# Kernel optimization log

Measured on AMD Instinct MI355X. Metric: run time of the kernel, lower is better.

## Reference

```python
import jax, jax.numpy as jnp
import numpy as np


def setup_inputs() -> dict:
    key = jax.random.key(0)
    k1, k2, k3, k4 = jax.random.split(key, 4)
    B, H, W, C, NCLS = 128, 14, 14, 512, 200
    # post-ReLU-like non-negative feature map
    x = jax.random.uniform(k1, (B, H, W, C), dtype=jnp.float32)
    # one-hot-like logits for ground-truth labels (only argmax is used)
    gt = jax.random.normal(k2, (B, NCLS), dtype=jnp.float32)
    # positional template codebook; index [H, W] (== shape[0]-1) is the sentinel
    # 'negative' template used for all-zero channels
    t_p = jax.random.normal(k3, (H + 1, W + 1, H, W), dtype=jnp.float32)
    # per-class channel template, broadcast-multiplied with masked features
    class_templates = jax.random.uniform(k4, (NCLS, H, W, C), dtype=jnp.float32)
    return {"x": x, "gt": gt, "t_p": t_p, "class_templates": class_templates}


def reference(x, gt, t_p, class_templates):
    # x: [B, H, W, C] channels-last feature map
    B, H, W, C = x.shape
    flat = x.reshape(B, H * W, C)
    # global spatial argmax per (batch, channel) == max_pool_with_argmax over full extent
    idx = jnp.argmax(flat, axis=1)            # [B, C]
    h = idx // W                               # [B, C]
    w = idx % W                                # [B, C]
    # channels whose spatial max is exactly 0 get the sentinel template index
    empty = jnp.max(flat, axis=1) == 0.0       # [B, C]
    sentinel = t_p.shape[0] - 1
    h = jnp.where(empty, sentinel, h)
    w = jnp.where(empty, sentinel, w)
    # gather positional templates: [B, C, H, W] -> [B, H, W, C]
    templates = jnp.transpose(t_p[h, w], (0, 2, 3, 1))
    masked = jax.nn.relu(x * templates)
    # training branch with gt, reduce_loss=False: mask by the class template
    cls = jnp.argmax(gt, axis=1)               # [B]
    masked = masked * class_templates[cls]     # [B, H, W, C]
    return (masked, x, templates)
```

## Files before the change

kernel.cpp:

```cpp
#include <hip/hip_runtime.h>

#define B    128
#define H    14
#define W    14
#define C    512
#define NCLS 200
#define HW   (H * W)
#define TP_DIM 15
#define SENT_OFF ((14 * TP_DIM + 14) * HW)

typedef float  v4f __attribute__((ext_vector_type(4)));
typedef int    v4i __attribute__((ext_vector_type(4)));

__global__ __launch_bounds__(512) void fused_kernel(
        const float* __restrict__ x,
        const float* __restrict__ gt,
        const float* __restrict__ t_p,
        const float* __restrict__ ctpl,
        float*       __restrict__ out) {
    __shared__ int s_off[C];
    __shared__ int s_cls;

    const int tid  = threadIdx.x;
    const int b    = blockIdx.x >> 1;
    const int half = blockIdx.x & 1;

    {
        const float* xp = x + (size_t)b * HW * C + tid;
        float best = xp[0];
        int   bs   = 0;
#pragma unroll 13
        for (int s = 1; s < HW; ++s) {
            float v = xp[(size_t)s * C];
            if (v > best) { best = v; bs = s; }
        }
        int off;
        if (best == 0.0f) {
            off = SENT_OFF;
        } else {
            int h = bs / W;
            int w = bs - h * W;
            off = (h * TP_DIM + w) * HW;
        }
        s_off[tid] = off;
    }

    if (tid < 64) {
        const float* g = gt + (size_t)b * NCLS;
        float gb = -__builtin_inff();
        int   gi = NCLS;
        for (int i = tid; i < NCLS; i += 64) {
            float v = g[i];
            if (v > gb) { gb = v; gi = i; }
        }
#pragma unroll
        for (int d = 1; d < 64; d <<= 1) {
            float ov = __shfl_xor(gb, d);
            int   oi = __shfl_xor(gi, d);
            if (ov > gb || (ov == gb && oi < gi)) { gb = ov; gi = oi; }
        }
        if (tid == 0) s_cls = gi;
    }

    __syncthreads();

    const int klass   = s_cls;
    const int q_base  = half ? 25 : 0;
    const int n_quads = half ? 24 : 25;
    const int n_tiles = n_quads * 128;

    const size_t plane = (size_t)B * HW * C;

    for (int e = tid; e < n_tiles; e += 512) {
        int cg = e & 127;
        int q  = e >> 7;
        int s0 = (q_base + q) * 4;
        int c0 = cg * 4;

        int o0 = s_off[c0 + 0];
        int o1 = s_off[c0 + 1];
        int o2 = s_off[c0 + 2];
        int o3 = s_off[c0 + 3];

        v4f t0 = *(const v4f*)(t_p + o0 + s0);
        v4f t1 = *(const v4f*)(t_p + o1 + s0);
        v4f t2 = *(const v4f*)(t_p + o2 + s0);
        v4f t3 = *(const v4f*)(t_p + o3 + s0);
        v4f tv[4];
        tv[0] = (v4f){t0.x, t1.x, t2.x, t3.x};
        tv[1] = (v4f){t0.y, t1.y, t2.y, t3.y};
        tv[2] = (v4f){t0.z, t1.z, t2.z, t3.z};
        tv[3] = (v4f){t0.w, t1.w, t2.w, t3.w};

        const size_t base = ((size_t)b * HW + s0) * C + c0;
        const float* __restrict__ xp = x + base;
        const float* __restrict__ cp = ctpl + ((size_t)klass * HW + s0) * C + c0;
        float* __restrict__ out_m = out + base;
        float* __restrict__ out_x = out + plane + base;
        float* __restrict__ out_t = out + 2 * plane + base;

#pragma unroll
        for (int i = 0; i < 4; ++i) {
            v4f xv = *(const v4f*)(xp + (size_t)i * C);
            v4f ct = *(const v4f*)(cp + (size_t)i * C);
            v4f t  = tv[i];
            v4f m;
            m.x = fmaxf(xv.x * t.x, 0.0f) * ct.x;
            m.y = fmaxf(xv.y * t.y, 0.0f) * ct.y;
            m.z = fmaxf(xv.z * t.z, 0.0f) * ct.z;
            m.w = fmaxf(xv.w * t.w, 0.0f) * ct.w;
            __builtin_nontemporal_store(m,  (v4f*)(out_m + (size_t)i * C));
            __builtin_nontemporal_store(xv, (v4f*)(out_x + (size_t)i * C));
            __builtin_nontemporal_store(t,  (v4f*)(out_t + (size_t)i * C));
        }
    }
}

extern "C" void kernel_launch(void* const* d_in, const int* in_sizes, int n_in,
                              void* d_out, int out_size, void* d_ws, size_t ws_size,
                              hipStream_t stream) {
    const float* x    = (const float*)d_in[0];
    const float* gt   = (const float*)d_in[1];
    const float* t_p  = (const float*)d_in[2];
    const float* ctpl = (const float*)d_in[3];
    float* out = (float*)d_out;

    hipLaunchKernelGGL(fused_kernel,
                       dim3(2 * B), dim3(512), 0, stream,
                       x, gt, t_p, ctpl, out);
}
```

Measured before the change: 265.9 us.

## Split argmax into separate kernel with parallel spatial reduction, then streaming kernel

The fused kernel is split into two launches. The first computes the per-channel spatial argmax, with 8 thread slices each reducing part of the spatial extent using vector loads, then a shared-memory merge; it also finds the class argmax and writes template offsets and class ids to workspace. The second kernel runs 1024 blocks of 256 threads and streams the masked, x and template outputs. This removes the redundant argmax that each half-block did before and the serial 196-step reduction per thread, and raises parallelism in the streaming phase. In exchange it adds a second launch, a round trip through global workspace, and a second read of x.

Result: slower. 272.4 us (+2.5%).

```diff
diff --git a/kernel.cpp b/kernel.cpp
--- a/kernel.cpp
+++ b/kernel.cpp
@@ -12,44 +12,65 @@
 typedef float  v4f __attribute__((ext_vector_type(4)));
 typedef int    v4i __attribute__((ext_vector_type(4)));
 
-__global__ __launch_bounds__(512) void fused_kernel(
+__global__ __launch_bounds__(512) void argmax_kernel(
         const float* __restrict__ x,
         const float* __restrict__ gt,
-        const float* __restrict__ t_p,
-        const float* __restrict__ ctpl,
-        float*       __restrict__ out) {
-    __shared__ int s_off[C];
-    __shared__ int s_cls;
+        int* __restrict__ ws_off,
+        int* __restrict__ ws_cls) {
+    __shared__ v4f s_best[8][64];
+    __shared__ v4i s_idx[8][64];
 
     const int tid  = threadIdx.x;
     const int b    = blockIdx.x >> 1;
     const int half = blockIdx.x & 1;
+    const int cg   = tid & 63;
+    const int sl   = tid >> 6;
+    const int c0   = half * 256 + cg * 4;
 
-    {
-        const float* xp = x + (size_t)b * HW * C + tid;
-        float best = xp[0];
-        int   bs   = 0;
-#pragma unroll 13
-        for (int s = 1; s < HW; ++s) {
-            float v = xp[(size_t)s * C];
-            if (v > best) { best = v; bs = s; }
-        }
-        int off;
-        if (best == 0.0f) {
-            off = SENT_OFF;
-        } else {
-            int h = bs / W;
-            int w = bs - h * W;
-            off = (h * TP_DIM + w) * HW;
-        }
-        s_off[tid] = off;
+    const int sbeg = sl * 25;
+    const int scnt = (sl == 7) ? (HW - 7 * 25) : 25;
+
+    const float* __restrict__ xp = x + (size_t)b * HW * C + c0;
+
+    v4f best = *(const v4f*)(xp + (size_t)sbeg * C);
+    v4i bidx = (v4i){sbeg, sbeg, sbeg, sbeg};
+#pragma unroll 4
+    for (int k = 1; k < scnt; ++k) {
+        const int s = sbeg + k;
+        v4f v = *(const v4f*)(xp + (size_t)s * C);
+        if (v.x > best.x) { best.x = v.x; bidx.x = s; }
+        if (v.y > best.y) { best.y = v.y; bidx.y = s; }
+        if (v.z > best.z) { best.z = v.z; bidx.z = s; }
+        if (v.w > best.w) { best.w = v.w; bidx.w = s; }
     }
+    s_best[sl][cg] = best;
+    s_idx[sl][cg]  = bidx;
+    __syncthreads();
 
     if (tid < 64) {
-        const float* g = gt + (size_t)b * NCLS;
+        v4f cb = s_best[0][tid];
+        v4i ci = s_idx[0][tid];
+#pragma unroll
+        for (int k = 1; k < 8; ++k) {
+            v4f p = s_best[k][tid];
+            v4i q = s_idx[k][tid];
+            if (p.x > cb.x) { cb.x = p.x; ci.x = q.x; }
+            if (p.y > cb.y) { cb.y = p.y; ci.y = q.y; }
+            if (p.z > cb.z) { cb.z = p.z; ci.z = q.z; }
+            if (p.w > cb.w) { cb.w = p.w; ci.w = q.w; }
+        }
+        v4i o;
+        o.x = (cb.x == 0.0f) ? SENT_OFF : ((ci.x / W) * TP_DIM + (ci.x % W)) * HW;
+        o.y = (cb.y == 0.0f) ? SENT_OFF : ((ci.y / W) * TP_DIM + (ci.y % W)) * HW;
+        o.z = (cb.z == 0.0f) ? SENT_OFF : ((ci.z / W) * TP_DIM + (ci.z % W)) * HW;
+        o.w = (cb.w == 0.0f) ? SENT_OFF : ((ci.w / W) * TP_DIM + (ci.w % W)) * HW;
+        *(v4i*)(ws_off + (size_t)b * C + half * 256 + tid * 4) = o;
+    } else if (half == 0 && tid < 128) {
+        const int lane = tid - 64;
+        const float* __restrict__ g = gt + (size_t)b * NCLS;
         float gb = -__builtin_inff();
         int   gi = NCLS;
-        for (int i = tid; i < NCLS; i += 64) {
+        for (int i = lane; i < NCLS; i += 64) {
             float v = g[i];
             if (v > gb) { gb = v; gi = i; }
         }
@@ -59,33 +80,37 @@
             int   oi = __shfl_xor(gi, d);
             if (ov > gb || (ov == gb && oi < gi)) { gb = ov; gi = oi; }
         }
-        if (tid == 0) s_cls = gi;
+        if (lane == 0) ws_cls[b] = gi;
     }
+}
 
-    __syncthreads();
-
-    const int klass   = s_cls;
-    const int q_base  = half ? 25 : 0;
-    const int n_quads = half ? 24 : 25;
-    const int n_tiles = n_quads * 128;
+__global__ __launch_bounds__(256) void stream_kernel(
+        const float* __restrict__ x,
+        const float* __restrict__ t_p,
+        const float* __restrict__ ctpl,
+        const int*   __restrict__ ws_off,
+        const int*   __restrict__ ws_cls,
+        float*       __restrict__ out) {
+    const int b     = blockIdx.x & 127;
+    const int chunk = blockIdx.x >> 7;
+    const int cls   = ws_cls[b];
 
     const size_t plane = (size_t)B * HW * C;
+    const int*   __restrict__ offp = ws_off + (size_t)b * C;
+    const float* __restrict__ ctp  = ctpl + (size_t)cls * HW * C;
 
-    for (int e = tid; e < n_tiles; e += 512) {
-        int cg = e & 127;
-        int q  = e >> 7;
-        int s0 = (q_base + q) * 4;
-        int c0 = cg * 4;
+    for (int t = chunk * 256 + (int)threadIdx.x; t < 49 * 128; t += 2048) {
+        const int q  = t >> 7;
+        const int cg = t & 127;
+        const int s0 = q * 4;
+        const int c0 = cg * 4;
 
-        int o0 = s_off[c0 + 0];
-        int o1 = s_off[c0 + 1];
-        int o2 = s_off[c0 + 2];
-        int o3 = s_off[c0 + 3];
+        v4i off = *(const v4i*)(offp + c0);
 
-        v4f t0 = *(const v4f*)(t_p + o0 + s0);
-        v4f t1 = *(const v4f*)(t_p + o1 + s0);
-        v4f t2 = *(const v4f*)(t_p + o2 + s0);
-        v4f t3 = *(const v4f*)(t_p + o3 + s0);
+        v4f t0 = *(const v4f*)(t_p + off.x + s0);
+        v4f t1 = *(const v4f*)(t_p + off.y + s0);
+        v4f t2 = *(const v4f*)(t_p + off.z + s0);
+        v4f t3 = *(const v4f*)(t_p + off.w + s0);
         v4f tv[4];
         tv[0] = (v4f){t0.x, t1.x, t2.x, t3.x};
         tv[1] = (v4f){t0.y, t1.y, t2.y, t3.y};
@@ -94,7 +119,7 @@
 
         const size_t base = ((size_t)b * HW + s0) * C + c0;
         const float* __restrict__ xp = x + base;
-        const float* __restrict__ cp = ctpl + ((size_t)klass * HW + s0) * C + c0;
+        const float* __restrict__ cp = ctp + (size_t)s0 * C + c0;
         float* __restrict__ out_m = out + base;
         float* __restrict__ out_x = out + plane + base;
         float* __restrict__ out_t = out + 2 * plane + base;
@@ -103,15 +128,15 @@
         for (int i = 0; i < 4; ++i) {
             v4f xv = *(const v4f*)(xp + (size_t)i * C);
             v4f ct = *(const v4f*)(cp + (size_t)i * C);
-            v4f t  = tv[i];
+            v4f tt = tv[i];
             v4f m;
-            m.x = fmaxf(xv.x * t.x, 0.0f) * ct.x;
-            m.y = fmaxf(xv.y * t.y, 0.0f) * ct.y;
-            m.z = fmaxf(xv.z * t.z, 0.0f) * ct.z;
-            m.w = fmaxf(xv.w * t.w, 0.0f) * ct.w;
+            m.x = fmaxf(xv.x * tt.x, 0.0f) * ct.x;
+            m.y = fmaxf(xv.y * tt.y, 0.0f) * ct.y;
+            m.z = fmaxf(xv.z * tt.z, 0.0f) * ct.z;
+            m.w = fmaxf(xv.w * tt.w, 0.0f) * ct.w;
             __builtin_nontemporal_store(m,  (v4f*)(out_m + (size_t)i * C));
             __builtin_nontemporal_store(xv, (v4f*)(out_x + (size_t)i * C));
-            __builtin_nontemporal_store(t,  (v4f*)(out_t + (size_t)i * C));
+            __builtin_nontemporal_store(tt, (v4f*)(out_t + (size_t)i * C));
         }
     }
 }
@@ -125,7 +150,13 @@
     const float* ctpl = (const float*)d_in[3];
     float* out = (float*)d_out;
 
-    hipLaunchKernelGGL(fused_kernel,
+    int* ws_off = (int*)d_ws;
+    int* ws_cls = ws_off + B * C;
+
+    hipLaunchKernelGGL(argmax_kernel,
                        dim3(2 * B), dim3(512), 0, stream,
-                       x, gt, t_p, ctpl, out);
+                       x, gt, ws_off, ws_cls);
+    hipLaunchKernelGGL(stream_kernel,
+                       dim3(8 * B), dim3(256), 0, stream,
+                       x, t_p, ctpl, ws_off, ws_cls, out);
 }
```
